# Kernel optimization log

Measured on AMD Instinct MI355X. Metric: run time of the kernel, lower is better.

The kernel has to match this reference:

```python
import jax, jax.numpy as jnp
import numpy as np

NUM_GRAPHS = 512  # number of distinct graph ids in batch


def _gcn_agg(x, batch):
    # mm(block_full_adj, x) == per-graph sum broadcast back to nodes
    sums = jax.ops.segment_sum(x, batch, num_segments=NUM_GRAPHS)
    return sums[batch]


def setup_inputs() -> dict:
    key = jax.random.key(0)
    ks = jax.random.split(key, 8)
    N, D = 100000, 128
    H = 2 * D
    x = jax.random.normal(ks[0], (N, D), dtype=jnp.float32)
    batch = jnp.sort(jax.random.randint(ks[1], (N,), 0, NUM_GRAPHS)).astype(jnp.int64)
    s = 0.05
    W1 = jax.random.normal(ks[2], (D, H), dtype=jnp.float32) * s
    b1 = jax.random.normal(ks[3], (H,), dtype=jnp.float32) * s
    W2 = jax.random.normal(ks[4], (H, H), dtype=jnp.float32) * s
    b2 = jax.random.normal(ks[5], (H,), dtype=jnp.float32) * s
    Wc = jax.random.normal(ks[6], (H, 1), dtype=jnp.float32) * s
    bc = jax.random.normal(ks[7], (1,), dtype=jnp.float32) * s
    return {"x": x, "batch": batch, "W1": W1, "b1": b1, "W2": W2, "b2": b2, "Wc": Wc, "bc": bc}


def reference(x, batch, W1, b1, W2, b2, Wc, bc):
    h = jax.nn.relu(_gcn_agg(x, batch) @ W1 + b1)          # GCN layer 1
    h = jax.nn.relu(_gcn_agg(h, batch) @ W2 + b2)          # GCN layer 2
    c = h @ Wc + bc                                         # confidence head
    sp = jax.nn.softplus(c)
    return sp / (1.0 + sp)
```

## Files before the change

kernel.cpp:

```cpp
#include <hip/hip_runtime.h>
#include <math.h>

#define NUM_GRAPHS 512
#define D 128
#define HDIM 256
#define K 8
#define GPB 2


__device__ __forceinline__ int detect_is64(const int* __restrict__ b, int N)
{
    const int j = ((N - 1) & 1) ? (N - 1) : (N - 2);
    return b[j] == 0;
}

__device__ __forceinline__ int wave_lower_bound(const int* __restrict__ b32,
                                                int is64, int N, int target,
                                                int lane)
{
    const long long* b64 = (const long long*)b32;
    int lo = 0, hi = N;
    while (hi > lo) {
        const int len  = hi - lo;
        const int step = (len + 63) >> 6;
        const int p    = lo + lane * step;
        int lt = 0;
        if (p < hi) {
            int v = is64 ? (int)b64[p] : b32[p];
            lt = (v < target);
        }
        unsigned long long m = __ballot(lt);
        int cnt = __popcll(m);
        if (cnt == 0) { hi = lo; break; }
        int nlo = lo + (cnt - 1) * step + 1;
        int nhi = min(lo + cnt * step, hi);
        lo = nlo; hi = nhi;
    }
    return lo;
}

__global__ __launch_bounds__(256) void seg_sum(
    const float* __restrict__ x, const int* __restrict__ batch32,
    float4* __restrict__ partial4, int* __restrict__ bounds, int N)
{
    const int blk  = blockIdx.x;
    const int g    = blk >> 3;
    const int k    = blk & 7;
    const int tid  = threadIdx.x;
    const int lane = tid & 63;
    const int wv   = tid >> 6;

    __shared__ int    sStart, sEnd;
    __shared__ float4 part[256];

    if (wv < 2) {
        const int is64 = detect_is64(batch32, N);
        int r = wave_lower_bound(batch32, is64, N, g + wv, lane);
        if (lane == 0) {
            if (wv == 0) sStart = r; else sEnd = r;
        }
    }
    __syncthreads();

    const int start = sStart, end = sEnd;
    if (k == 0 && tid == 0) {
        bounds[g] = start;
        if (g == NUM_GRAPHS - 1) bounds[NUM_GRAPHS] = end;
    }

    const int n   = end - start;
    const int per = (n + K - 1) / K;
    const int r0  = start + k * per;
    const int r1  = min(r0 + per, end);

    const int r  = tid >> 5;
    const int c4 = tid & 31;
    float4 a0 = make_float4(0.f, 0.f, 0.f, 0.f);
    float4 a1 = make_float4(0.f, 0.f, 0.f, 0.f);
    const float4* x4 = (const float4*)x;
    int row = r0 + r;
    for (; row + 8 < r1; row += 16) {
        float4 v0 = x4[row * 32 + c4];
        float4 v1 = x4[(row + 8) * 32 + c4];
        a0.x += v0.x; a0.y += v0.y; a0.z += v0.z; a0.w += v0.w;
        a1.x += v1.x; a1.y += v1.y; a1.z += v1.z; a1.w += v1.w;
    }
    if (row < r1) {
        float4 v0 = x4[row * 32 + c4];
        a0.x += v0.x; a0.y += v0.y; a0.z += v0.z; a0.w += v0.w;
    }
    a0.x += a1.x; a0.y += a1.y; a0.z += a1.z; a0.w += a1.w;

    part[tid] = a0;
    __syncthreads();
    for (int s = 4; s >= 1; s >>= 1) {
        if (r < s) {
            float4 o = part[tid + s * 32];
            float4 m = part[tid];
            m.x += o.x; m.y += o.y; m.z += o.z; m.w += o.w;
            part[tid] = m;
        }
        __syncthreads();
    }
    if (tid < 32)
        partial4[blk * 32 + tid] = part[tid];
}

__global__ __launch_bounds__(256) void mlp_scatter(
    const float* __restrict__ partial, const int* __restrict__ bounds,
    const float* __restrict__ W1, const float* __restrict__ b1,
    const float* __restrict__ W2, const float* __restrict__ b2,
    const float* __restrict__ Wc, const float* __restrict__ bc,
    float* __restrict__ out)
{
    const int g0  = blockIdx.x * GPB;
    const int tid = threadIdx.x;

    __shared__ int   sBound[GPB + 1];
    __shared__ float sS[GPB][D];
    __shared__ float sH[GPB][HDIM];
    __shared__ float sRed[4][GPB];
    __shared__ float sCval[GPB];

    if (tid <= GPB) sBound[tid] = bounds[g0 + tid];

    {
        const int j = tid >> 7;
        const int dcol = tid & (D - 1);
        float s = 0.f;
        #pragma unroll
        for (int k = 0; k < K; ++k)
            s += partial[((g0 + j) * K + k) * D + dcol];
        sS[j][dcol] = s;
    }
    __syncthreads();

    float a1[GPB];
    {
        float bb = b1[tid];
        #pragma unroll
        for (int j = 0; j < GPB; ++j) a1[j] = bb;
    }
    #pragma unroll 16
    for (int k = 0; k < D; ++k) {
        float w = W1[k * HDIM + tid];
        #pragma unroll
        for (int j = 0; j < GPB; ++j) a1[j] = fmaf(sS[j][k], w, a1[j]);
    }
    #pragma unroll
    for (int j = 0; j < GPB; ++j) {
        float cnt = (float)(sBound[j + 1] - sBound[j]);
        sH[j][tid] = fmaxf(a1[j], 0.f) * cnt;
    }
    __syncthreads();

    float a2[GPB];
    {
        float bb = b2[tid];
        #pragma unroll
        for (int j = 0; j < GPB; ++j) a2[j] = bb;
    }
    #pragma unroll 16
    for (int k = 0; k < HDIM; ++k) {
        float w = W2[k * HDIM + tid];
        #pragma unroll
        for (int j = 0; j < GPB; ++j) a2[j] = fmaf(sH[j][k], w, a2[j]);
    }
    float wc = Wc[tid];
    float v[GPB];
    #pragma unroll
    for (int j = 0; j < GPB; ++j) v[j] = fmaxf(a2[j], 0.f) * wc;
    for (int off = 32; off > 0; off >>= 1) {
        #pragma unroll
        for (int j = 0; j < GPB; ++j) v[j] += __shfl_down(v[j], off, 64);
    }
    if ((tid & 63) == 0) {
        #pragma unroll
        for (int j = 0; j < GPB; ++j) sRed[tid >> 6][j] = v[j];
    }
    __syncthreads();
    if (tid < GPB) {
        float cc = sRed[0][tid] + sRed[1][tid] + sRed[2][tid] + sRed[3][tid]
                 + bc[0];
        float m  = fmaxf(cc, 0.f);
        float sp = m + log1pf(expf(-fabsf(cc)));
        sCval[tid] = sp / (1.f + sp);
    }
    __syncthreads();

    {
        const int s0 = sBound[0], s1 = sBound[1], s2 = sBound[GPB];
        const float v0 = sCval[0], v1 = sCval[1];
        for (int i = s0 + tid; i < s2; i += 256)
            out[i] = (i < s1) ? v0 : v1;
    }
}

extern "C" void kernel_launch(void* const* d_in, const int* in_sizes, int n_in,
                              void* d_out, int out_size, void* d_ws, size_t ws_size,
                              hipStream_t stream)
{
    const float* x   = (const float*)d_in[0];
    const int*   bat = (const int*)d_in[1];
    const float* W1  = (const float*)d_in[2];
    const float* b1  = (const float*)d_in[3];
    const float* W2  = (const float*)d_in[4];
    const float* b2  = (const float*)d_in[5];
    const float* Wc  = (const float*)d_in[6];
    const float* bc  = (const float*)d_in[7];
    float* out = (float*)d_out;
    const int N = in_sizes[0] / D;

    int*   bounds  = (int*)d_ws;
    float* partial = (float*)((char*)d_ws + 4096);

    seg_sum<<<NUM_GRAPHS * K, 256, 0, stream>>>(x, bat, (float4*)partial,
                                                bounds, N);
    mlp_scatter<<<NUM_GRAPHS / GPB, 256, 0, stream>>>(partial, bounds,
                                                      W1, b1, W2, b2, Wc, bc,
                                                      out);
}
```

Before: 111.7 us.

## Fuse segment sum and per-graph MLP into one kernel, one block per graph

Merges the segment-sum kernel and the MLP/scatter kernel into a single kernel where each block handles one graph end to end. This removes the second launch and the global round trip for partial sums and bounds. It also adds four-way unrolled nontemporal loads when reading x. The cost is parallelism: the reduction now runs on 512 blocks instead of 4096, so each block reads about 195 rows serially and the weight reads are no longer shared across two graphs per block.

```diff
diff --git a/kernel.cpp b/kernel.cpp
--- a/kernel.cpp
+++ b/kernel.cpp
@@ -4,8 +4,8 @@
 #define NUM_GRAPHS 512
 #define D 128
 #define HDIM 256
-#define K 8
-#define GPB 2
+
+typedef float f4 __attribute__((ext_vector_type(4)));
 
 
 __device__ __forceinline__ int detect_is64(const int* __restrict__ b, int N)
@@ -39,161 +39,93 @@
     return lo;
 }
 
-__global__ __launch_bounds__(256) void seg_sum(
+__global__ __launch_bounds__(256) void fused_gcn(
     const float* __restrict__ x, const int* __restrict__ batch32,
-    float4* __restrict__ partial4, int* __restrict__ bounds, int N)
+    const float* __restrict__ W1, const float* __restrict__ b1,
+    const float* __restrict__ W2, const float* __restrict__ b2,
+    const float* __restrict__ Wc, const float* __restrict__ bc,
+    float* __restrict__ out, int N)
 {
-    const int blk  = blockIdx.x;
-    const int g    = blk >> 3;
-    const int k    = blk & 7;
+    const int g    = blockIdx.x;
     const int tid  = threadIdx.x;
     const int lane = tid & 63;
     const int wv   = tid >> 6;
 
-    __shared__ int    sStart, sEnd;
-    __shared__ float4 part[256];
+    __shared__ int   sStart, sEnd;
+    __shared__ f4    part[256];
+    __shared__ float sH[HDIM];
+    __shared__ float sRed[4];
+    __shared__ float sCval;
 
     if (wv < 2) {
         const int is64 = detect_is64(batch32, N);
         int r = wave_lower_bound(batch32, is64, N, g + wv, lane);
-        if (lane == 0) {
-            if (wv == 0) sStart = r; else sEnd = r;
-        }
+        if (lane == 0) { if (wv == 0) sStart = r; else sEnd = r; }
     }
     __syncthreads();
 
     const int start = sStart, end = sEnd;
-    if (k == 0 && tid == 0) {
-        bounds[g] = start;
-        if (g == NUM_GRAPHS - 1) bounds[NUM_GRAPHS] = end;
-    }
-
-    const int n   = end - start;
-    const int per = (n + K - 1) / K;
-    const int r0  = start + k * per;
-    const int r1  = min(r0 + per, end);
 
     const int r  = tid >> 5;
     const int c4 = tid & 31;
-    float4 a0 = make_float4(0.f, 0.f, 0.f, 0.f);
-    float4 a1 = make_float4(0.f, 0.f, 0.f, 0.f);
-    const float4* x4 = (const float4*)x;
-    int row = r0 + r;
-    for (; row + 8 < r1; row += 16) {
-        float4 v0 = x4[row * 32 + c4];
-        float4 v1 = x4[(row + 8) * 32 + c4];
-        a0.x += v0.x; a0.y += v0.y; a0.z += v0.z; a0.w += v0.w;
-        a1.x += v1.x; a1.y += v1.y; a1.z += v1.z; a1.w += v1.w;
+    const f4* x4 = (const f4*)x;
+    f4 a0 = (f4){0.f, 0.f, 0.f, 0.f};
+    f4 a1 = (f4){0.f, 0.f, 0.f, 0.f};
+    f4 a2 = (f4){0.f, 0.f, 0.f, 0.f};
+    f4 a3 = (f4){0.f, 0.f, 0.f, 0.f};
+    int row = start + r;
+    for (; row + 24 < end; row += 32) {
+        f4 v0 = __builtin_nontemporal_load(&x4[row * 32 + c4]);
+        f4 v1 = __builtin_nontemporal_load(&x4[(row + 8) * 32 + c4]);
+        f4 v2 = __builtin_nontemporal_load(&x4[(row + 16) * 32 + c4]);
+        f4 v3 = __builtin_nontemporal_load(&x4[(row + 24) * 32 + c4]);
+        a0 += v0; a1 += v1; a2 += v2; a3 += v3;
     }
-    if (row < r1) {
-        float4 v0 = x4[row * 32 + c4];
-        a0.x += v0.x; a0.y += v0.y; a0.z += v0.z; a0.w += v0.w;
+    for (; row < end; row += 8) {
+        f4 v0 = __builtin_nontemporal_load(&x4[row * 32 + c4]);
+        a0 += v0;
     }
-    a0.x += a1.x; a0.y += a1.y; a0.z += a1.z; a0.w += a1.w;
+    a0 += a1 + a2 + a3;
 
     part[tid] = a0;
     __syncthreads();
     for (int s = 4; s >= 1; s >>= 1) {
         if (r < s) {
-            float4 o = part[tid + s * 32];
-            float4 m = part[tid];
-            m.x += o.x; m.y += o.y; m.z += o.z; m.w += o.w;
-            part[tid] = m;
+            part[tid] += part[tid + s * 32];
         }
         __syncthreads();
     }
-    if (tid < 32)
-        partial4[blk * 32 + tid] = part[tid];
-}
+    const float* sS = (const float*)part;
 
-__global__ __launch_bounds__(256) void mlp_scatter(
-    const float* __restrict__ partial, const int* __restrict__ bounds,
-    const float* __restrict__ W1, const float* __restrict__ b1,
-    const float* __restrict__ W2, const float* __restrict__ b2,
-    const float* __restrict__ Wc, const float* __restrict__ bc,
-    float* __restrict__ out)
-{
-    const int g0  = blockIdx.x * GPB;
-    const int tid = threadIdx.x;
+    float acc1 = b1[tid];
+    #pragma unroll 16
+    for (int k = 0; k < D; ++k)
+        acc1 = fmaf(sS[k], W1[k * HDIM + tid], acc1);
+    const float cnt = (float)(end - start);
+    sH[tid] = fmaxf(acc1, 0.f) * cnt;
+    __syncthreads();
 
-    __shared__ int   sBound[GPB + 1];
-    __shared__ float sS[GPB][D];
-    __shared__ float sH[GPB][HDIM];
-    __shared__ float sRed[4][GPB];
-    __shared__ float sCval[GPB];
+    float acc2 = b2[tid];
+    #pragma unroll 16
+    for (int k = 0; k < HDIM; ++k)
+        acc2 = fmaf(sH[k], W2[k * HDIM + tid], acc2);
 
-    if (tid <= GPB) sBound[tid] = bounds[g0 + tid];
-
-    {
-        const int j = tid >> 7;
-        const int dcol = tid & (D - 1);
-        float s = 0.f;
-        #pragma unroll
-        for (int k = 0; k < K; ++k)
-            s += partial[((g0 + j) * K + k) * D + dcol];
-        sS[j][dcol] = s;
+    float v = fmaxf(acc2, 0.f) * Wc[tid];
+    for (int off = 32; off > 0; off >>= 1)
+        v += __shfl_down(v, off, 64);
+    if (lane == 0) sRed[wv] = v;
+    __syncthreads();
+    if (tid == 0) {
+        float cc = sRed[0] + sRed[1] + sRed[2] + sRed[3] + bc[0];
+        float m  = fmaxf(cc, 0.f);
+        float sp = m + log1pf(expf(-fabsf(cc)));
+        sCval = sp / (1.f + sp);
     }
     __syncthreads();
 
-    float a1[GPB];
-    {
-        float bb = b1[tid];
-        #pragma unroll
-        for (int j = 0; j < GPB; ++j) a1[j] = bb;
-    }
-    #pragma unroll 16
-    for (int k = 0; k < D; ++k) {
-        float w = W1[k * HDIM + tid];
-        #pragma unroll
-        for (int j = 0; j < GPB; ++j) a1[j] = fmaf(sS[j][k], w, a1[j]);
-    }
-    #pragma unroll
-    for (int j = 0; j < GPB; ++j) {
-        float cnt = (float)(sBound[j + 1] - sBound[j]);
-        sH[j][tid] = fmaxf(a1[j], 0.f) * cnt;
-    }
-    __syncthreads();
-
-    float a2[GPB];
-    {
-        float bb = b2[tid];
-        #pragma unroll
-        for (int j = 0; j < GPB; ++j) a2[j] = bb;
-    }
-    #pragma unroll 16
-    for (int k = 0; k < HDIM; ++k) {
-        float w = W2[k * HDIM + tid];
-        #pragma unroll
-        for (int j = 0; j < GPB; ++j) a2[j] = fmaf(sH[j][k], w, a2[j]);
-    }
-    float wc = Wc[tid];
-    float v[GPB];
-    #pragma unroll
-    for (int j = 0; j < GPB; ++j) v[j] = fmaxf(a2[j], 0.f) * wc;
-    for (int off = 32; off > 0; off >>= 1) {
-        #pragma unroll
-        for (int j = 0; j < GPB; ++j) v[j] += __shfl_down(v[j], off, 64);
-    }
-    if ((tid & 63) == 0) {
-        #pragma unroll
-        for (int j = 0; j < GPB; ++j) sRed[tid >> 6][j] = v[j];
-    }
-    __syncthreads();
-    if (tid < GPB) {
-        float cc = sRed[0][tid] + sRed[1][tid] + sRed[2][tid] + sRed[3][tid]
-                 + bc[0];
-        float m  = fmaxf(cc, 0.f);
-        float sp = m + log1pf(expf(-fabsf(cc)));
-        sCval[tid] = sp / (1.f + sp);
-    }
-    __syncthreads();
-
-    {
-        const int s0 = sBound[0], s1 = sBound[1], s2 = sBound[GPB];
-        const float v0 = sCval[0], v1 = sCval[1];
-        for (int i = s0 + tid; i < s2; i += 256)
-            out[i] = (i < s1) ? v0 : v1;
-    }
+    const float val = sCval;
+    for (int i = start + tid; i < end; i += 256)
+        out[i] = val;
 }
 
 extern "C" void kernel_launch(void* const* d_in, const int* in_sizes, int n_in,
@@ -211,12 +143,8 @@
     float* out = (float*)d_out;
     const int N = in_sizes[0] / D;
 
-    int*   bounds  = (int*)d_ws;
-    float* partial = (float*)((char*)d_ws + 4096);
+    (void)d_ws; (void)ws_size;
 
-    seg_sum<<<NUM_GRAPHS * K, 256, 0, stream>>>(x, bat, (float4*)partial,
-                                                bounds, N);
-    mlp_scatter<<<NUM_GRAPHS / GPB, 256, 0, stream>>>(partial, bounds,
-                                                      W1, b1, W2, b2, Wc, bc,
-                                                      out);
+    fused_gcn<<<NUM_GRAPHS, 256, 0, stream>>>(x, bat, W1, b1, W2, b2, Wc, bc,
+                                              out, N);
 }
```

After: 111.5 us. About the same (-0.1%).
